# Optimization experiments

Measured on AMD Instinct MI355X. Metric: run time of the kernel, lower is better.

## Reference

```python
import jax, jax.numpy as jnp
import numpy as np

B, BITS, HID = 4096, 64, 512
EPS = 1e-5
TEMPERATURE = 1.0  # buffer default


def _w(k, shape):
    return jax.random.normal(k, shape, jnp.float32) * 0.02


def setup_inputs() -> dict:
    key = jax.random.key(0)
    ks = jax.random.split(key, 8)
    return {
        "a_bits": jax.random.uniform(ks[0], (B, BITS), jnp.float32),
        "shift_bits": jax.random.uniform(ks[1], (B, BITS), jnp.float32),
        # shift_decoder params
        "W1": _w(ks[2], (HID, BITS)), "b1": jnp.zeros((HID,), jnp.float32),
        "g1": jnp.ones((HID,), jnp.float32), "be1": jnp.zeros((HID,), jnp.float32),
        "W2": _w(ks[3], (HID, HID)), "b2": jnp.zeros((HID,), jnp.float32),
        "g2": jnp.ones((HID,), jnp.float32), "be2": jnp.zeros((HID,), jnp.float32),
        "W3": _w(ks[4], (BITS, HID)), "b3": jnp.zeros((BITS,), jnp.float32),
        # index_net params (input dim = 2*BITS)
        "Wi1": _w(ks[5], (HID, 2 * BITS)), "bi1": jnp.zeros((HID,), jnp.float32),
        "Wi2": _w(ks[6], (HID, HID)), "bi2": jnp.zeros((HID,), jnp.float32),
        "Wi3": _w(ks[7], (BITS, HID)), "bi3": jnp.zeros((BITS,), jnp.float32),
    }


def _layernorm(x, g, b):
    m = jnp.mean(x, axis=-1, keepdims=True)
    v = jnp.mean(jnp.square(x - m), axis=-1, keepdims=True)
    return (x - m) * jax.lax.rsqrt(v + EPS) * g + b


def reference(a_bits, shift_bits, W1, b1, g1, be1, W2, b2, g2, be2, W3, b3,
              Wi1, bi1, Wi2, bi2, Wi3, bi3):
    # shift decoder: Linear -> LN -> ReLU -> Linear -> LN -> ReLU -> Linear
    h = jax.nn.relu(_layernorm(shift_bits @ W1.T + b1, g1, be1))
    h = jax.nn.relu(_layernorm(h @ W2.T + b2, g2, be2))
    shift_logits = h @ W3.T + b3                        # [B, BITS]
    shift_soft = jax.nn.softmax(shift_logits / TEMPERATURE, axis=-1)

    # index_net, vectorized over the output-position loop.
    # combined = [one_hot(i), shift_soft]; the one-hot part of the first Linear
    # just selects column i of Wi1[:, :BITS], so we add it as a [BITS, HID] bias.
    pos_part = Wi1[:, :BITS].T                          # [BITS, HID]
    shift_part = shift_soft @ Wi1[:, BITS:].T           # [B, HID]
    h1 = jax.nn.relu(pos_part[None, :, :] + shift_part[:, None, :] + bi1)  # [B, BITS, HID]
    h2 = jax.nn.relu(jnp.einsum('bph,kh->bpk', h1, Wi2) + bi2)             # [B, BITS, HID]
    idx_logits = jnp.einsum('bph,kh->bpk', h2, Wi3) + bi3                  # [B, BITS, BITS]
    idx_soft = jax.nn.softmax(idx_logits / TEMPERATURE, axis=-1)

    # softmax-weighted gather-sum over a_bits
    return jnp.einsum('bpj,bj->bp', idx_soft, a_bits)   # [B, BITS]
```

## Files before the change

kernel.cpp:

```cpp
#include <hip/hip_runtime.h>
#include <hip/hip_bf16.h>
#include <math.h>

#define B_N 4096
#define BITSN 64
#define HID 512
#define EPSV 1e-5f
#define BT 16

typedef unsigned short ushort_t;
typedef __attribute__((ext_vector_type(8))) short bf16x8;
typedef __attribute__((ext_vector_type(4))) float f32x4;
typedef __attribute__((ext_vector_type(16))) float f32x16;

__device__ __forceinline__ ushort_t f2bf(float f) {
  unsigned u = __float_as_uint(f);
  u += 0x7FFF + ((u >> 16) & 1);
  return (ushort_t)(u >> 16);
}

__device__ __forceinline__ unsigned pack2bf(float lo, float hi) {
  union { __hip_bfloat162 h; unsigned u; } cv;
  cv.h = __float22bfloat162_rn(make_float2(lo, hi));
  return cv.u;
}

__device__ __forceinline__ float bf2f(short v) {
  return __uint_as_float(((unsigned)(unsigned short)v) << 16);
}

__global__ __launch_bounds__(256) void prep_kernel(
    const float* __restrict__ Wi2, const float* __restrict__ Wi3,
    const float* __restrict__ Wi1, const float* __restrict__ W1,
    const float* __restrict__ W2, const float* __restrict__ W3,
    ushort_t* __restrict__ Wi1posTb, ushort_t* __restrict__ W1b,
    ushort_t* __restrict__ W2f, ushort_t* __restrict__ W3b,
    ushort_t* __restrict__ Wi1sb, ushort_t* __restrict__ Wi2f32,
    ushort_t* __restrict__ Wi3f) {
  int idx = blockIdx.x * 256 + threadIdx.x;
  if (idx < 512 * 512) {
    {
      int j = idx & 7, lane = (idx >> 3) & 63;
      int ct = (idx >> 9) & 31, ks = idx >> 14;
      int c = ct * 16 + (lane & 15);
      int k = ks * 32 + (lane >> 4) * 8 + j;
      W2f[idx] = f2bf(W2[c * 512 + k]);
    }
    {
      int j = idx & 7, lane = (idx >> 3) & 63;
      int ct = (idx >> 9) & 15, ks = idx >> 13;
      int c = ct * 32 + (lane & 31);
      int k = ks * 16 + (lane >> 5) * 8 + j;
      Wi2f32[idx] = f2bf(Wi2[c * 512 + k]);
    }
  }
  if (idx < 64 * 512) {
    W3b[idx] = f2bf(W3[idx]);
    int p = idx >> 9, i = idx & 511;
    Wi1posTb[idx] = f2bf(Wi1[i * 128 + p]);
    int j = idx & 7, lane = (idx >> 3) & 63;
    int nt = (idx >> 9) & 3, ks2 = idx >> 11;
    int jr = nt * 16 + (lane & 15);
    int k = ks2 * 32 + (lane >> 4) * 8 + j;
    Wi3f[idx] = f2bf(Wi3[jr * 512 + k]);
  }
  if (idx < 512 * 64) {
    W1b[idx] = f2bf(W1[idx]);
    int j = idx >> 6, k = idx & 63;
    Wi1sb[idx] = f2bf(Wi1[j * 128 + 64 + k]);
  }
}

__global__ __launch_bounds__(256) void shift2_kernel(
    const float* __restrict__ shift_bits,
    const ushort_t* __restrict__ W1b, const float* __restrict__ b1,
    const float* __restrict__ g1, const float* __restrict__ be1,
    const ushort_t* __restrict__ W2f, const float* __restrict__ b2,
    const float* __restrict__ g2, const float* __restrict__ be2,
    const ushort_t* __restrict__ W3b, const float* __restrict__ b3,
    const ushort_t* __restrict__ Wi1sb, const float* __restrict__ bi1,
    float* __restrict__ sp) {
  __shared__ __align__(16) ushort_t hA[BT * 512];
  __shared__ __align__(16) char reg2[32 * 1024];
  __shared__ float b1s[512], g1s[512], be1s[512];
  __shared__ float b2s[512], g2s[512], be2s[512], bi1s[512];
  __shared__ float red[4][BT][2];
  __shared__ float b3s[64];

  ushort_t* sbt = (ushort_t*)reg2;
  ushort_t* h2  = (ushort_t*)reg2;
  float (*lg32)[68] = (float(*)[68])(reg2 + 16 * 1024);
  ushort_t* sb2 = (ushort_t*)(reg2 + 16 * 1024 + 16 * 68 * 4);

  int b0 = blockIdx.x * BT;
  int t = threadIdx.x, w = t >> 6, l = t & 63, lg = l >> 4, l15 = l & 15;

  b1s[t] = b1[t];  b1s[t + 256] = b1[t + 256];
  g1s[t] = g1[t];  g1s[t + 256] = g1[t + 256];
  be1s[t] = be1[t]; be1s[t + 256] = be1[t + 256];
  b2s[t] = b2[t];  b2s[t + 256] = b2[t + 256];
  g2s[t] = g2[t];  g2s[t + 256] = g2[t + 256];
  be2s[t] = be2[t]; be2s[t + 256] = be2[t + 256];
  bi1s[t] = bi1[t]; bi1s[t + 256] = bi1[t + 256];
  if (t < 64) b3s[t] = b3[t];
  if (t < 128) {
    int row = t >> 3, g = t & 7;
    const float* src = shift_bits + (size_t)(b0 + row) * 64 + g * 8;
    uint4 pk;
    pk.x = (unsigned)f2bf(src[0]) | ((unsigned)f2bf(src[1]) << 16);
    pk.y = (unsigned)f2bf(src[2]) | ((unsigned)f2bf(src[3]) << 16);
    pk.z = (unsigned)f2bf(src[4]) | ((unsigned)f2bf(src[5]) << 16);
    pk.w = (unsigned)f2bf(src[6]) | ((unsigned)f2bf(src[7]) << 16);
    *(uint4*)((char*)sbt + ((row * 128 + g * 16) ^ ((row & 7) << 4))) = pk;
  }
  __syncthreads();

  f32x4 acc[8];
#pragma unroll
  for (int nt = 0; nt < 8; ++nt) acc[nt] = (f32x4){0.f, 0.f, 0.f, 0.f};
#pragma unroll
  for (int ks = 0; ks < 2; ++ks) {
    bf16x8 af = *(const bf16x8*)((char*)sbt + ((l15 * 128 + ks * 64 + lg * 16) ^ ((l15 & 7) << 4)));
#pragma unroll
    for (int nt = 0; nt < 8; ++nt) {
      int c = w * 128 + nt * 16 + l15;
      bf16x8 bfr = *(const bf16x8*)(W1b + (size_t)c * 64 + ks * 32 + lg * 8);
      acc[nt] = __builtin_amdgcn_mfma_f32_16x16x32_bf16(af, bfr, acc[nt], 0, 0, 0);
    }
  }
  {
    float s[4] = {0.f, 0.f, 0.f, 0.f}, q[4] = {0.f, 0.f, 0.f, 0.f};
#pragma unroll
    for (int nt = 0; nt < 8; ++nt) {
      int c = w * 128 + nt * 16 + l15;
      float bb = b1s[c];
#pragma unroll
      for (int r = 0; r < 4; ++r) {
        float x = acc[nt][r] + bb;
        acc[nt][r] = x;
        s[r] += x; q[r] += x * x;
      }
    }
#pragma unroll
    for (int m = 8; m >= 1; m >>= 1)
#pragma unroll
      for (int r = 0; r < 4; ++r) { s[r] += __shfl_xor(s[r], m); q[r] += __shfl_xor(q[r], m); }
    if (l15 == 0)
#pragma unroll
      for (int r = 0; r < 4; ++r) { red[w][4 * lg + r][0] = s[r]; red[w][4 * lg + r][1] = q[r]; }
    __syncthreads();
    float mean[4], rs[4];
#pragma unroll
    for (int r = 0; r < 4; ++r) {
      int p = 4 * lg + r;
      float S = red[0][p][0] + red[1][p][0] + red[2][p][0] + red[3][p][0];
      float Q = red[0][p][1] + red[1][p][1] + red[2][p][1] + red[3][p][1];
      mean[r] = S * (1.0f / 512.0f);
      float var = Q * (1.0f / 512.0f) - mean[r] * mean[r];
      rs[r] = rsqrtf(var + EPSV);
    }
#pragma unroll
    for (int nt = 0; nt < 8; ++nt) {
      int c = w * 128 + nt * 16 + l15;
      float gg = g1s[c], bb = be1s[c];
#pragma unroll
      for (int r = 0; r < 4; ++r) {
        int p = 4 * lg + r;
        float v = (acc[nt][r] - mean[r]) * rs[r] * gg + bb;
        v = v > 0.f ? v : 0.f;
        *(ushort_t*)((char*)hA + ((p * 1024 + c * 2) ^ ((p & 7) << 4))) = f2bf(v);
      }
    }
  }
  __syncthreads();

#pragma unroll
  for (int nt = 0; nt < 8; ++nt) acc[nt] = (f32x4){0.f, 0.f, 0.f, 0.f};
  {
    const bf16x8* w2base = (const bf16x8*)W2f + ((size_t)(w * 8) * 64 + l);
#pragma unroll 2
    for (int step = 0; step < 16; ++step) {
      bf16x8 af = *(const bf16x8*)((char*)hA + ((l15 * 1024 + step * 64 + lg * 16) ^ ((l15 & 7) << 4)));
#pragma unroll
      for (int nt = 0; nt < 8; ++nt) {
        bf16x8 bfr = w2base[((size_t)step * 32 + nt) * 64];
        acc[nt] = __builtin_amdgcn_mfma_f32_16x16x32_bf16(af, bfr, acc[nt], 0, 0, 0);
      }
    }
  }
  __syncthreads();
  {
    float s[4] = {0.f, 0.f, 0.f, 0.f}, q[4] = {0.f, 0.f, 0.f, 0.f};
#pragma unroll
    for (int nt = 0; nt < 8; ++nt) {
      int c = w * 128 + nt * 16 + l15;
      float bb = b2s[c];
#pragma unroll
      for (int r = 0; r < 4; ++r) {
        float x = acc[nt][r] + bb;
        acc[nt][r] = x;
        s[r] += x; q[r] += x * x;
      }
    }
#pragma unroll
    for (int m = 8; m >= 1; m >>= 1)
#pragma unroll
      for (int r = 0; r < 4; ++r) { s[r] += __shfl_xor(s[r], m); q[r] += __shfl_xor(q[r], m); }
    if (l15 == 0)
#pragma unroll
      for (int r = 0; r < 4; ++r) { red[w][4 * lg + r][0] = s[r]; red[w][4 * lg + r][1] = q[r]; }
    __syncthreads();
    float mean[4], rs[4];
#pragma unroll
    for (int r = 0; r < 4; ++r) {
      int p = 4 * lg + r;
      float S = red[0][p][0] + red[1][p][0] + red[2][p][0] + red[3][p][0];
      float Q = red[0][p][1] + red[1][p][1] + red[2][p][1] + red[3][p][1];
      mean[r] = S * (1.0f / 512.0f);
      float var = Q * (1.0f / 512.0f) - mean[r] * mean[r];
      rs[r] = rsqrtf(var + EPSV);
    }
#pragma unroll
    for (int nt = 0; nt < 8; ++nt) {
      int c = w * 128 + nt * 16 + l15;
      float gg = g2s[c], bb = be2s[c];
#pragma unroll
      for (int r = 0; r < 4; ++r) {
        int p = 4 * lg + r;
        float v = (acc[nt][r] - mean[r]) * rs[r] * gg + bb;
        v = v > 0.f ? v : 0.f;
        *(ushort_t*)((char*)h2 + ((p * 1024 + c * 2) ^ ((p & 7) << 4))) = f2bf(v);
      }
    }
  }
  __syncthreads();

  {
    f32x4 a3 = (f32x4){0.f, 0.f, 0.f, 0.f};
#pragma unroll
    for (int ks = 0; ks < 16; ++ks) {
      bf16x8 af = *(const bf16x8*)((char*)h2 + ((l15 * 1024 + ks * 64 + lg * 16) ^ ((l15 & 7) << 4)));
      bf16x8 bfr = *(const bf16x8*)(W3b + (size_t)(w * 16 + l15) * 512 + ks * 32 + lg * 8);
      a3 = __builtin_amdgcn_mfma_f32_16x16x32_bf16(af, bfr, a3, 0, 0, 0);
    }
    int c = w * 16 + l15;
    float bb = b3s[c];
#pragma unroll
    for (int r = 0; r < 4; ++r) lg32[4 * lg + r][c] = a3[r] + bb;
  }
  __syncthreads();

  {
    int r = t >> 4, j = t & 15;
    float v[4];
    float m = -1e30f;
#pragma unroll
    for (int mq = 0; mq < 4; ++mq) { v[mq] = lg32[r][mq * 16 + j]; m = fmaxf(m, v[mq]); }
#pragma unroll
    for (int mk = 8; mk >= 1; mk >>= 1) m = fmaxf(m, __shfl_xor(m, mk));
    float ssum = 0.f;
#pragma unroll
    for (int mq = 0; mq < 4; ++mq) { v[mq] = expf(v[mq] - m); ssum += v[mq]; }
#pragma unroll
    for (int mk = 8; mk >= 1; mk >>= 1) ssum += __shfl_xor(ssum, mk);
    float inv = 1.f / ssum;
#pragma unroll
    for (int mq = 0; mq < 4; ++mq) {
      int c = mq * 16 + j;
      *(ushort_t*)((char*)sb2 + ((r * 128 + c * 2) ^ ((r & 7) << 4))) = f2bf(v[mq] * inv);
    }
  }
  __syncthreads();

  {
    f32x4 a4[8];
#pragma unroll
    for (int nt = 0; nt < 8; ++nt) a4[nt] = (f32x4){0.f, 0.f, 0.f, 0.f};
#pragma unroll
    for (int ks = 0; ks < 2; ++ks) {
      bf16x8 af = *(const bf16x8*)((char*)sb2 + ((l15 * 128 + ks * 64 + lg * 16) ^ ((l15 & 7) << 4)));
#pragma unroll
      for (int nt = 0; nt < 8; ++nt) {
        int c = w * 128 + nt * 16 + l15;
        bf16x8 bfr = *(const bf16x8*)(Wi1sb + (size_t)c * 64 + ks * 32 + lg * 8);
        a4[nt] = __builtin_amdgcn_mfma_f32_16x16x32_bf16(af, bfr, a4[nt], 0, 0, 0);
      }
    }
#pragma unroll
    for (int nt = 0; nt < 8; ++nt) {
      int c = w * 128 + nt * 16 + l15;
      float bb = bi1s[c];
#pragma unroll
      for (int r = 0; r < 4; ++r)
        sp[(size_t)(b0 + 4 * lg + r) * 512 + c] = a4[nt][r] + bb;
    }
  }
}

__global__ __launch_bounds__(512, 4) void big10_kernel(
    const float* __restrict__ a_bits, const float* __restrict__ sp,
    const ushort_t* __restrict__ posTb,
    const ushort_t* __restrict__ Wi2f32, const ushort_t* __restrict__ Wi3f,
    const float* __restrict__ bi2, const float* __restrict__ bi3,
    float* __restrict__ out) {
  __shared__ __align__(16) ushort_t h1s[64 * 512];
  __shared__ float bi2s[512];
  __shared__ float ab[64];
  __shared__ float bi3s[64];

  int b = blockIdx.x, t = threadIdx.x;
  int w = t >> 6, l = t & 63;
  int l31 = l & 31, hi = l >> 5;
  int lg = l >> 4, l15 = l & 15;

  bi2s[t] = bi2[t];
  if (t < 64) { ab[t] = a_bits[b * 64 + t]; bi3s[t] = bi3[t]; }

  {
    const float* sprow = sp + (size_t)b * 512 + l * 8;
    float4 s0 = *(const float4*)(sprow);
    float4 s1 = *(const float4*)(sprow + 4);
#pragma unroll
    for (int g = 0; g < 8; ++g) {
      int p = g * 8 + w;
      bf16x8 pr = *(const bf16x8*)(posTb + (size_t)p * 512 + l * 8);
      float v0 = fmaxf(s0.x + bf2f(pr[0]), 0.f), v1 = fmaxf(s0.y + bf2f(pr[1]), 0.f);
      float v2 = fmaxf(s0.z + bf2f(pr[2]), 0.f), v3 = fmaxf(s0.w + bf2f(pr[3]), 0.f);
      float v4 = fmaxf(s1.x + bf2f(pr[4]), 0.f), v5 = fmaxf(s1.y + bf2f(pr[5]), 0.f);
      float v6 = fmaxf(s1.z + bf2f(pr[6]), 0.f), v7 = fmaxf(s1.w + bf2f(pr[7]), 0.f);
      uint4 pk;
      pk.x = pack2bf(v0, v1); pk.y = pack2bf(v2, v3);
      pk.z = pack2bf(v4, v5); pk.w = pack2bf(v6, v7);
      *(uint4*)((char*)h1s + ((p * 1024 + l * 16) ^ ((p & 15) << 4))) = pk;
    }
  }
  __syncthreads();

  f32x16 acc[2][2];
#pragma unroll
  for (int mc = 0; mc < 2; ++mc)
#pragma unroll
    for (int np = 0; np < 2; ++np)
#pragma unroll
      for (int r = 0; r < 16; ++r) acc[mc][np][r] = 0.f;

  {
    const bf16x8* bbase = (const bf16x8*)Wi2f32 + ((size_t)(2 * w) * 64 + l);
    bf16x8 wf[4][2];
#pragma unroll
    for (int d = 0; d < 4; ++d) {
      wf[d][0] = bbase[(size_t)d * 1024];
      wf[d][1] = bbase[(size_t)d * 1024 + 64];
    }
    for (int kb = 0; kb < 8; ++kb) {
#pragma unroll
      for (int d = 0; d < 4; ++d) {
        int ks = kb * 4 + d;
        bf16x8 w0 = wf[d][0], w1 = wf[d][1];
        if (kb < 7) {
          wf[d][0] = bbase[(size_t)(ks + 4) * 1024];
          wf[d][1] = bbase[(size_t)(ks + 4) * 1024 + 64];
        }
        int row0 = l31, row1 = 32 + l31;
        bf16x8 h0 = *(const bf16x8*)((char*)h1s + ((row0 * 1024 + ks * 32 + hi * 16) ^ ((row0 & 15) << 4)));
        bf16x8 h1v = *(const bf16x8*)((char*)h1s + ((row1 * 1024 + ks * 32 + hi * 16) ^ ((row1 & 15) << 4)));
        __builtin_amdgcn_s_setprio(1);
        acc[0][0] = __builtin_amdgcn_mfma_f32_32x32x16_bf16(w0, h0, acc[0][0], 0, 0, 0);
        acc[0][1] = __builtin_amdgcn_mfma_f32_32x32x16_bf16(w0, h1v, acc[0][1], 0, 0, 0);
        acc[1][0] = __builtin_amdgcn_mfma_f32_32x32x16_bf16(w1, h0, acc[1][0], 0, 0, 0);
        acc[1][1] = __builtin_amdgcn_mfma_f32_32x32x16_bf16(w1, h1v, acc[1][1], 0, 0, 0);
        __builtin_amdgcn_s_setprio(0);
      }
    }
  }
  __syncthreads();

#pragma unroll
  for (int mc = 0; mc < 2; ++mc) {
#pragma unroll
    for (int np = 0; np < 2; ++np) {
      int p = np * 32 + l31;
#pragma unroll
      for (int rq = 0; rq < 4; ++rq) {
        int c0 = w * 64 + mc * 32 + 8 * rq + 4 * hi;
        float4 bi4 = *(const float4*)(bi2s + c0);
        float v0 = fmaxf(acc[mc][np][4 * rq + 0] + bi4.x, 0.f);
        float v1 = fmaxf(acc[mc][np][4 * rq + 1] + bi4.y, 0.f);
        float v2 = fmaxf(acc[mc][np][4 * rq + 2] + bi4.z, 0.f);
        float v3 = fmaxf(acc[mc][np][4 * rq + 3] + bi4.w, 0.f);
        uint2 pk;
        pk.x = pack2bf(v0, v1);
        pk.y = pack2bf(v2, v3);
        *(uint2*)((char*)h1s + ((p * 1024 + c0 * 2) ^ ((p & 15) << 4))) = pk;
      }
    }
  }
  __syncthreads();

  f32x4 lacc[2];
  lacc[0] = (f32x4){0.f, 0.f, 0.f, 0.f};
  lacc[1] = (f32x4){0.f, 0.f, 0.f, 0.f};
  {
    int pw = w >> 1, jh = w & 1;
    int p2 = 16 * pw + l15;
    const bf16x8* b3base = (const bf16x8*)Wi3f + l;
#pragma unroll 4
    for (int ks2 = 0; ks2 < 16; ++ks2) {
      bf16x8 a2 = *(const bf16x8*)((char*)h1s + ((p2 * 1024 + ks2 * 64 + lg * 16) ^ ((p2 & 15) << 4)));
      bf16x8 g0 = b3base[(ks2 * 4 + 2 * jh + 0) * 64];
      bf16x8 g1 = b3base[(ks2 * 4 + 2 * jh + 1) * 64];
      __builtin_amdgcn_s_setprio(1);
      lacc[0] = __builtin_amdgcn_mfma_f32_16x16x32_bf16(a2, g0, lacc[0], 0, 0, 0);
      lacc[1] = __builtin_amdgcn_mfma_f32_16x16x32_bf16(a2, g1, lacc[1], 0, 0, 0);
      __builtin_amdgcn_s_setprio(0);
    }
  }
  __syncthreads();

  {
    float* Lg = (float*)h1s;
    int pw = w >> 1, jh = w & 1;
#pragma unroll
    for (int q = 0; q < 2; ++q) {
      int j = (2 * jh + q) * 16 + l15;
#pragma unroll
      for (int r = 0; r < 4; ++r) {
        int p = pw * 16 + 4 * lg + r;
        Lg[p * 68 + j] = lacc[q][r];
      }
    }
  }
  __syncthreads();

  {
    const float* Lg = (const float*)h1s;
    int p = t >> 3, jo = t & 7;
    float s = 0.f, g = 0.f;
#pragma unroll
    for (int m = 0; m < 8; ++m) {
      int c = jo * 8 + m;
      float e = __expf(Lg[p * 68 + c] + bi3s[c]);
      s += e; g += e * ab[c];
    }
#pragma unroll
    for (int mm = 4; mm >= 1; mm >>= 1) { s += __shfl_xor(s, mm); g += __shfl_xor(g, mm); }
    if (jo == 0) out[b * 64 + p] = g / s;
  }
}

extern "C" void kernel_launch(void* const* d_in, const int* in_sizes, int n_in,
                              void* d_out, int out_size, void* d_ws, size_t ws_size,
                              hipStream_t stream) {
  const float* a_bits     = (const float*)d_in[0];
  const float* shift_bits = (const float*)d_in[1];
  const float* W1  = (const float*)d_in[2];
  const float* b1  = (const float*)d_in[3];
  const float* g1  = (const float*)d_in[4];
  const float* be1 = (const float*)d_in[5];
  const float* W2  = (const float*)d_in[6];
  const float* b2  = (const float*)d_in[7];
  const float* g2  = (const float*)d_in[8];
  const float* be2 = (const float*)d_in[9];
  const float* W3  = (const float*)d_in[10];
  const float* b3  = (const float*)d_in[11];
  const float* Wi1 = (const float*)d_in[12];
  const float* bi1 = (const float*)d_in[13];
  const float* Wi2 = (const float*)d_in[14];
  const float* bi2 = (const float*)d_in[15];
  const float* Wi3 = (const float*)d_in[16];
  const float* bi3 = (const float*)d_in[17];
  float* out = (float*)d_out;

  float* sp = (float*)d_ws;
  ushort_t* W2f = (ushort_t*)((char*)d_ws + (size_t)B_N * HID * 4);
  ushort_t* W1b = W2f + 512 * 512;
  ushort_t* W3b = W1b + 512 * 64;
  ushort_t* Wi1sb = W3b + 64 * 512;
  ushort_t* Wi1posTb = Wi1sb + 512 * 64;
  ushort_t* Wi2f32 = Wi1posTb + 64 * 512;
  ushort_t* Wi3f = Wi2f32 + 512 * 512;

  prep_kernel<<<1024, 256, 0, stream>>>(Wi2, Wi3, Wi1, W1, W2, W3,
                                        Wi1posTb, W1b, W2f, W3b, Wi1sb, Wi2f32, Wi3f);
  shift2_kernel<<<B_N / BT, 256, 0, stream>>>(shift_bits, W1b, b1, g1, be1,
                                              W2f, b2, g2, be2, W3b, b3, Wi1sb, bi1, sp);
  big10_kernel<<<B_N, 512, 0, stream>>>(a_bits, sp, Wi1posTb, Wi2f32, Wi3f, bi2, bi3, out);
}
```

Measured before the change: 202.2 us.

## Split index-net block into two 32-position halves with 256 threads

Each batch row is now handled by two 256-thread blocks, one per half of the 64 output positions, instead of one 512-thread block. The Wi2 GEMM is rearranged so each wave computes four 32-column tiles against one 32-row A fragment, with double-buffered weight fragments. Halving shared memory per block is meant to raise occupancy and the number of resident blocks per CU. The cost is that each Wi2/Wi3 weight fragment is reused across half as many positions, so weight reads from L2 roughly double.

```diff
diff --git a/kernel.cpp b/kernel.cpp
--- a/kernel.cpp
+++ b/kernel.cpp
@@ -297,33 +297,34 @@
   }
 }
 
-__global__ __launch_bounds__(512, 4) void big10_kernel(
+__global__ __launch_bounds__(256, 4) void big11_kernel(
     const float* __restrict__ a_bits, const float* __restrict__ sp,
     const ushort_t* __restrict__ posTb,
     const ushort_t* __restrict__ Wi2f32, const ushort_t* __restrict__ Wi3f,
     const float* __restrict__ bi2, const float* __restrict__ bi3,
     float* __restrict__ out) {
-  __shared__ __align__(16) ushort_t h1s[64 * 512];
+  __shared__ __align__(16) ushort_t h1s[32 * 512];
   __shared__ float bi2s[512];
   __shared__ float ab[64];
   __shared__ float bi3s[64];
 
-  int b = blockIdx.x, t = threadIdx.x;
+  int bid = blockIdx.x, t = threadIdx.x;
+  int B = bid >> 1, H = bid & 1, prow0 = H * 32;
   int w = t >> 6, l = t & 63;
   int l31 = l & 31, hi = l >> 5;
   int lg = l >> 4, l15 = l & 15;
 
-  bi2s[t] = bi2[t];
-  if (t < 64) { ab[t] = a_bits[b * 64 + t]; bi3s[t] = bi3[t]; }
-
-  {
-    const float* sprow = sp + (size_t)b * 512 + l * 8;
+  bi2s[t] = bi2[t]; bi2s[t + 256] = bi2[t + 256];
+  if (t < 64) { ab[t] = a_bits[B * 64 + t]; bi3s[t] = bi3[t]; }
+
+  {
+    const float* sprow = sp + (size_t)B * 512 + l * 8;
     float4 s0 = *(const float4*)(sprow);
     float4 s1 = *(const float4*)(sprow + 4);
 #pragma unroll
     for (int g = 0; g < 8; ++g) {
-      int p = g * 8 + w;
-      bf16x8 pr = *(const bf16x8*)(posTb + (size_t)p * 512 + l * 8);
+      int p = g * 4 + w;
+      bf16x8 pr = *(const bf16x8*)(posTb + (size_t)(prow0 + p) * 512 + l * 8);
       float v0 = fmaxf(s0.x + bf2f(pr[0]), 0.f), v1 = fmaxf(s0.y + bf2f(pr[1]), 0.f);
       float v2 = fmaxf(s0.z + bf2f(pr[2]), 0.f), v3 = fmaxf(s0.w + bf2f(pr[3]), 0.f);
       float v4 = fmaxf(s1.x + bf2f(pr[4]), 0.f), v5 = fmaxf(s1.y + bf2f(pr[5]), 0.f);
@@ -336,63 +337,61 @@
   }
   __syncthreads();
 
-  f32x16 acc[2][2];
-#pragma unroll
-  for (int mc = 0; mc < 2; ++mc)
-#pragma unroll
-    for (int np = 0; np < 2; ++np)
-#pragma unroll
-      for (int r = 0; r < 16; ++r) acc[mc][np][r] = 0.f;
-
-  {
-    const bf16x8* bbase = (const bf16x8*)Wi2f32 + ((size_t)(2 * w) * 64 + l);
-    bf16x8 wf[4][2];
-#pragma unroll
-    for (int d = 0; d < 4; ++d) {
-      wf[d][0] = bbase[(size_t)d * 1024];
-      wf[d][1] = bbase[(size_t)d * 1024 + 64];
-    }
-    for (int kb = 0; kb < 8; ++kb) {
-#pragma unroll
-      for (int d = 0; d < 4; ++d) {
-        int ks = kb * 4 + d;
-        bf16x8 w0 = wf[d][0], w1 = wf[d][1];
-        if (kb < 7) {
-          wf[d][0] = bbase[(size_t)(ks + 4) * 1024];
-          wf[d][1] = bbase[(size_t)(ks + 4) * 1024 + 64];
-        }
-        int row0 = l31, row1 = 32 + l31;
-        bf16x8 h0 = *(const bf16x8*)((char*)h1s + ((row0 * 1024 + ks * 32 + hi * 16) ^ ((row0 & 15) << 4)));
-        bf16x8 h1v = *(const bf16x8*)((char*)h1s + ((row1 * 1024 + ks * 32 + hi * 16) ^ ((row1 & 15) << 4)));
+  f32x16 acc[4];
+#pragma unroll
+  for (int ct = 0; ct < 4; ++ct)
+#pragma unroll
+    for (int r = 0; r < 16; ++r) acc[ct][r] = 0.f;
+
+  {
+    const bf16x8* bbase = (const bf16x8*)Wi2f32 + ((size_t)(4 * w) * 64 + l);
+    bf16x8 wfA[4], wfB[4];
+#pragma unroll
+    for (int n = 0; n < 4; ++n) wfA[n] = bbase[n * 64];
+    for (int ks = 0; ks < 32; ks += 2) {
+#pragma unroll
+      for (int n = 0; n < 4; ++n) wfB[n] = bbase[(size_t)(ks + 1) * 1024 + n * 64];
+      {
+        bf16x8 a0 = *(const bf16x8*)((char*)h1s + ((l31 * 1024 + ks * 32 + hi * 16) ^ ((l31 & 15) << 4)));
         __builtin_amdgcn_s_setprio(1);
-        acc[0][0] = __builtin_amdgcn_mfma_f32_32x32x16_bf16(w0, h0, acc[0][0], 0, 0, 0);
-        acc[0][1] = __builtin_amdgcn_mfma_f32_32x32x16_bf16(w0, h1v, acc[0][1], 0, 0, 0);
-        acc[1][0] = __builtin_amdgcn_mfma_f32_32x32x16_bf16(w1, h0, acc[1][0], 0, 0, 0);
-        acc[1][1] = __builtin_amdgcn_mfma_f32_32x32x16_bf16(w1, h1v, acc[1][1], 0, 0, 0);
+        acc[0] = __builtin_amdgcn_mfma_f32_32x32x16_bf16(wfA[0], a0, acc[0], 0, 0, 0);
+        acc[1] = __builtin_amdgcn_mfma_f32_32x32x16_bf16(wfA[1], a0, acc[1], 0, 0, 0);
+        acc[2] = __builtin_amdgcn_mfma_f32_32x32x16_bf16(wfA[2], a0, acc[2], 0, 0, 0);
+        acc[3] = __builtin_amdgcn_mfma_f32_32x32x16_bf16(wfA[3], a0, acc[3], 0, 0, 0);
         __builtin_amdgcn_s_setprio(0);
       }
-    }
-  }
-  __syncthreads();
-
-#pragma unroll
-  for (int mc = 0; mc < 2; ++mc) {
-#pragma unroll
-    for (int np = 0; np < 2; ++np) {
-      int p = np * 32 + l31;
-#pragma unroll
-      for (int rq = 0; rq < 4; ++rq) {
-        int c0 = w * 64 + mc * 32 + 8 * rq + 4 * hi;
-        float4 bi4 = *(const float4*)(bi2s + c0);
-        float v0 = fmaxf(acc[mc][np][4 * rq + 0] + bi4.x, 0.f);
-        float v1 = fmaxf(acc[mc][np][4 * rq + 1] + bi4.y, 0.f);
-        float v2 = fmaxf(acc[mc][np][4 * rq + 2] + bi4.z, 0.f);
-        float v3 = fmaxf(acc[mc][np][4 * rq + 3] + bi4.w, 0.f);
-        uint2 pk;
-        pk.x = pack2bf(v0, v1);
-        pk.y = pack2bf(v2, v3);
-        *(uint2*)((char*)h1s + ((p * 1024 + c0 * 2) ^ ((p & 15) << 4))) = pk;
-      }
+      if (ks < 30) {
+#pragma unroll
+        for (int n = 0; n < 4; ++n) wfA[n] = bbase[(size_t)(ks + 2) * 1024 + n * 64];
+      }
+      {
+        bf16x8 a1 = *(const bf16x8*)((char*)h1s + ((l31 * 1024 + (ks + 1) * 32 + hi * 16) ^ ((l31 & 15) << 4)));
+        __builtin_amdgcn_s_setprio(1);
+        acc[0] = __builtin_amdgcn_mfma_f32_32x32x16_bf16(wfB[0], a1, acc[0], 0, 0, 0);
+        acc[1] = __builtin_amdgcn_mfma_f32_32x32x16_bf16(wfB[1], a1, acc[1], 0, 0, 0);
+        acc[2] = __builtin_amdgcn_mfma_f32_32x32x16_bf16(wfB[2], a1, acc[2], 0, 0, 0);
+        acc[3] = __builtin_amdgcn_mfma_f32_32x32x16_bf16(wfB[3], a1, acc[3], 0, 0, 0);
+        __builtin_amdgcn_s_setprio(0);
+      }
+    }
+  }
+  __syncthreads();
+
+#pragma unroll
+  for (int ct = 0; ct < 4; ++ct) {
+    int p = l31;
+#pragma unroll
+    for (int rq = 0; rq < 4; ++rq) {
+      int c0 = w * 128 + ct * 32 + 8 * rq + 4 * hi;
+      float4 bi4 = *(const float4*)(bi2s + c0);
+      float v0 = fmaxf(acc[ct][4 * rq + 0] + bi4.x, 0.f);
+      float v1 = fmaxf(acc[ct][4 * rq + 1] + bi4.y, 0.f);
+      float v2 = fmaxf(acc[ct][4 * rq + 2] + bi4.z, 0.f);
+      float v3 = fmaxf(acc[ct][4 * rq + 3] + bi4.w, 0.f);
+      uint2 pk;
+      pk.x = pack2bf(v0, v1);
+      pk.y = pack2bf(v2, v3);
+      *(uint2*)((char*)h1s + ((p * 1024 + c0 * 2) ^ ((p & 15) << 4))) = pk;
     }
   }
   __syncthreads();
@@ -401,8 +400,8 @@
   lacc[0] = (f32x4){0.f, 0.f, 0.f, 0.f};
   lacc[1] = (f32x4){0.f, 0.f, 0.f, 0.f};
   {
-    int pw = w >> 1, jh = w & 1;
-    int p2 = 16 * pw + l15;
+    int pt = w >> 1, jh = w & 1;
+    int p2 = 16 * pt + l15;
     const bf16x8* b3base = (const bf16x8*)Wi3f + l;
 #pragma unroll 4
     for (int ks2 = 0; ks2 < 16; ++ks2) {
@@ -419,13 +418,13 @@
 
   {
     float* Lg = (float*)h1s;
-    int pw = w >> 1, jh = w & 1;
+    int pt = w >> 1, jh = w & 1;
 #pragma unroll
     for (int q = 0; q < 2; ++q) {
       int j = (2 * jh + q) * 16 + l15;
 #pragma unroll
       for (int r = 0; r < 4; ++r) {
-        int p = pw * 16 + 4 * lg + r;
+        int p = pt * 16 + 4 * lg + r;
         Lg[p * 68 + j] = lacc[q][r];
       }
     }
@@ -444,7 +443,7 @@
     }
 #pragma unroll
     for (int mm = 4; mm >= 1; mm >>= 1) { s += __shfl_xor(s, mm); g += __shfl_xor(g, mm); }
-    if (jo == 0) out[b * 64 + p] = g / s;
+    if (jo == 0) out[B * 64 + prow0 + p] = g / s;
   }
 }
 
@@ -484,5 +483,5 @@
                                         Wi1posTb, W1b, W2f, W3b, Wi1sb, Wi2f32, Wi3f);
   shift2_kernel<<<B_N / BT, 256, 0, stream>>>(shift_bits, W1b, b1, g1, be1,
                                               W2f, b2, g2, be2, W3b, b3, Wi1sb, bi1, sp);
-  big10_kernel<<<B_N, 512, 0, stream>>>(a_bits, sp, Wi1posTb, Wi2f32, Wi3f, bi2, bi3, out);
-}
+  big11_kernel<<<B_N * 2, 256, 0, stream>>>(a_bits, sp, Wi1posTb, Wi2f32, Wi3f, bi2, bi3, out);
+}
```

After: 234.1 us. 15.8% more time.
